# Kernel optimization log

Hardware: AMD Instinct MI355X
Metric: run time of the kernel (lower is better)

Reference implementation:

```python
import jax, jax.numpy as jnp
import numpy as np

K = 512   # cardinality of each hidden source
O = 8     # n_out per party
NS = 3    # number of sources (triangle network)


def setup_inputs() -> dict:
    key = jax.random.key(0)
    k1, k2 = jax.random.split(key)
    n_pred = NS * K + 3 * K * K * O
    y_pred = jax.random.uniform(k1, (1, n_pred), dtype=jnp.float32)
    y_true = jax.random.uniform(k2, (O ** 3,), dtype=jnp.float32)
    y_true = y_true / jnp.sum(y_true)  # a proper target distribution
    return {"y_pred": y_pred, "y_true": y_true}


def _distribution(y_pred):
    # sources block: [NS, K] source probability tables
    srcs = y_pred[0, :NS * K].reshape(NS, K)
    pf = y_pred[0, NS * K:]
    sz = K * K * O
    # party response tensors, indexed by the two source symbols the party sees
    A = pf[:sz].reshape(K, K, O)          # A sees (beta, gamma) -> (j, k)
    B = pf[sz:2 * sz].reshape(K, K, O)    # B sees (gamma, alpha) -> (k, i)
    C = pf[2 * sz:].reshape(K, K, O)      # C sees (alpha, beta) -> (i, j)
    Pa, Pb, Pc = srcs[0], srcs[1], srcs[2]
    # prob[x,y,z] = sum_{i,j,k} Pa[i] Pb[j] Pc[k] A[j,k,x] B[k,i,y] C[i,j,z]
    Aw = A * Pb[:, None, None] * Pc[None, :, None]   # [j,k,x]
    Bw = B * Pa[None, :, None]                        # [k,i,y]
    T = jnp.einsum('jkx,kiy->ijxy', Aw, Bw)           # contract k; [K,K,O,O]
    probs = jnp.einsum('ijxy,ijz->xyz', T, C)         # contract i,j; [O,O,O]
    return probs.reshape(-1)


def reference(y_pred, y_true):
    probs = _distribution(y_pred)
    log_p = jnp.log(jnp.clip(probs, 1e-10, 1.0))
    d = jnp.sum(y_true * (jnp.log(y_true + 1e-10) - log_p))
    return (d, probs)
```

## Files before the change

### kernel.cpp

```cpp
#include <hip/hip_runtime.h>
#include <hip/hip_bf16.h>
#include <stdint.h>

#define KD 512
#define OD 8
#define SZ (KD*KD*OD)
#define PLANE (KD*KD)

typedef short v8s __attribute__((ext_vector_type(8)));
typedef float v4f __attribute__((ext_vector_type(4)));

static __device__ __forceinline__ unsigned short f2bf(float f) {
    union { float f; unsigned int u; } v; v.f = f;
    unsigned int u = v.u;
    unsigned int r = u + 0x7FFF + ((u >> 16) & 1);
    return (unsigned short)(r >> 16);
}


__global__ __launch_bounds__(256) void pack_kernel(const float* __restrict__ yp,
                                                   unsigned short* __restrict__ Wbf,
                                                   unsigned short* __restrict__ Xbf,
                                                   float* __restrict__ probs_acc) {
    __shared__ unsigned short lds[8 * 32 * 32];
    const float* Pa = yp;
    const float* Pb = yp + KD;
    const float* Pc = yp + 2 * KD;
    const float* A  = yp + 3 * KD;
    const float* B  = A + SZ;
    const int b = blockIdx.x;
    const int t = threadIdx.x;

    if (b == 0) { probs_acc[t] = 0.0f; probs_acc[t + 256] = 0.0f; }

    if (b < 256) {
        #pragma unroll
        for (int jj = 0; jj < 2; ++jj) {
            const int j = b * 2 + jj;
            const float pb = Pb[j];
            const int k0 = 2 * t;
            const float4* src = (const float4*)(A + ((size_t)j * KD + k0) * 8);
            float av[16];
            ((float4*)av)[0] = src[0];
            ((float4*)av)[1] = src[1];
            ((float4*)av)[2] = src[2];
            ((float4*)av)[3] = src[3];
            const float s0 = pb * Pc[k0];
            const float s1 = pb * Pc[k0 + 1];
            const size_t fo = (size_t)(k0 >> 5) * 16384 + (size_t)(j >> 4) * 512
                            + (size_t)((k0 >> 3) & 3) * 128 + (j & 15) * 8 + (k0 & 7);
            #pragma unroll
            for (int x = 0; x < 8; ++x) {
                ushort2 w;
                w.x = f2bf(av[x] * s0);
                w.y = f2bf(av[8 + x] * s1);
                *(ushort2*)(Wbf + (size_t)x * PLANE + fo) = w;
            }
        }
    } else {
        const int tb = b - 256;
        const int k0 = (tb / 16) * 32;
        const int i0 = (tb % 16) * 32;
        char* ldsb = (char*)lds;
        #pragma unroll
        for (int p = 0; p < 4; ++p) {
            const int idx = t + p * 256;
            const int dk = idx >> 5;
            const int di = idx & 31;
            const float pa = Pa[i0 + di];
            const float4* src = (const float4*)(B + ((size_t)(k0 + dk) * KD + (i0 + di)) * 8);
            float bv[8];
            ((float4*)bv)[0] = src[0];
            ((float4*)bv)[1] = src[1];
            const int swz = (di & 7) << 4;
            #pragma unroll
            for (int y = 0; y < 8; ++y)
                *(unsigned short*)(ldsb + (y * 32 + di) * 64 + ((dk * 2) ^ swz)) =
                    f2bf(bv[y] * pa);
        }
        __syncthreads();
        #pragma unroll
        for (int p = 0; p < 4; ++p) {
            const int c = t + p * 256;
            const int y = c >> 7;
            const int rem = c & 127;
            const int di = rem >> 2;
            const int dk8 = (rem & 3) * 8;
            uint4 v = *(const uint4*)(ldsb + (y * 32 + di) * 64 + ((dk8 * 2) ^ ((di & 7) << 4)));
            const size_t fo = (size_t)(k0 >> 5) * 16384 + (size_t)((i0 + di) >> 4) * 512
                            + (size_t)(dk8 >> 3) * 128 + (di & 15) * 8;
            *(uint4*)(Xbf + (size_t)y * PLANE + fo) = v;
        }
    }
}

__global__ __launch_bounds__(256, 4) void gemm_kernel(const float* __restrict__ yp,
                                                      const unsigned short* __restrict__ Wbf,
                                                      const unsigned short* __restrict__ Xbf,
                                                      float* __restrict__ probs_acc) {
    __shared__ float red[4][32];

    const int bid = blockIdx.x;
    const int xcd = bid & 7;
    const int local = bid >> 3;
    const int tl = local >> 4;
    const int group = local & 15;
    const int i_t = ((xcd >> 1) << 1) | (tl >> 2);
    const int j_t = ((xcd & 1) << 2) | (tl & 3);
    const int i0 = i_t * 64, j0 = j_t * 64;
    const int x0 = (group >> 2) * 2, y0 = (group & 3) * 2;

    const int t = threadIdx.x;
    const int w = t >> 6;
    const int l = t & 63;
    const int wm = w >> 1, wn = w & 1;
    const int lm = l & 15, quad = l >> 4;

    const unsigned short* aP[2];
    const unsigned short* bP[2];
    #pragma unroll
    for (int dy = 0; dy < 2; ++dy)
        aP[dy] = Xbf + (size_t)(y0 + dy) * PLANE
               + (size_t)((i0 + wm * 32) >> 4) * 512 + l * 8;
    #pragma unroll
    for (int dx = 0; dx < 2; ++dx)
        bP[dx] = Wbf + (size_t)(x0 + dx) * PLANE
               + (size_t)((j0 + wn * 32) >> 4) * 512 + l * 8;

    v4f acc[2][2][2][2];
    #pragma unroll
    for (int a = 0; a < 2; ++a)
      #pragma unroll
      for (int bb = 0; bb < 2; ++bb)
        #pragma unroll
        for (int c = 0; c < 2; ++c)
          #pragma unroll
          for (int d = 0; d < 2; ++d)
            acc[a][bb][c][d] = (v4f){0.f, 0.f, 0.f, 0.f};

    #pragma unroll 4
    for (int kt = 0; kt < 16; ++kt) {
        const int kof = kt * 16384;
        v8s aF[2][2], bF[2][2];
        #pragma unroll
        for (int dy = 0; dy < 2; ++dy)
            #pragma unroll
            for (int mt = 0; mt < 2; ++mt)
                aF[dy][mt] = *(const v8s*)(aP[dy] + kof + mt * 512);
        #pragma unroll
        for (int dx = 0; dx < 2; ++dx)
            #pragma unroll
            for (int nt = 0; nt < 2; ++nt)
                bF[dx][nt] = *(const v8s*)(bP[dx] + kof + nt * 512);
        #pragma unroll
        for (int dy = 0; dy < 2; ++dy)
            #pragma unroll
            for (int dx = 0; dx < 2; ++dx)
                #pragma unroll
                for (int mt = 0; mt < 2; ++mt)
                    #pragma unroll
                    for (int nt = 0; nt < 2; ++nt)
                        acc[dy][dx][mt][nt] = __builtin_amdgcn_mfma_f32_16x16x32_bf16(
                            aF[dy][mt], bF[dx][nt], acc[dy][dx][mt][nt], 0, 0, 0);
    }

    const float* Cp = yp + 3 * KD + 2 * (size_t)SZ;
    float zacc[2][2][8];
    #pragma unroll
    for (int dy = 0; dy < 2; ++dy)
      #pragma unroll
      for (int dx = 0; dx < 2; ++dx)
        #pragma unroll
        for (int z = 0; z < 8; ++z) zacc[dy][dx][z] = 0.f;

    #pragma unroll
    for (int mt = 0; mt < 2; ++mt) {
        #pragma unroll
        for (int nt = 0; nt < 2; ++nt) {
            #pragma unroll
            for (int r = 0; r < 4; ++r) {
                const int gi = i0 + wm * 32 + mt * 16 + quad * 4 + r;
                const int gj = j0 + wn * 32 + nt * 16 + lm;
                const float4* cp = (const float4*)(Cp + ((size_t)gi * KD + gj) * 8);
                const float4 c0 = cp[0], c1 = cp[1];
                #pragma unroll
                for (int dy = 0; dy < 2; ++dy) {
                    #pragma unroll
                    for (int dx = 0; dx < 2; ++dx) {
                        const float tv = acc[dy][dx][mt][nt][r];
                        zacc[dy][dx][0] += tv * c0.x; zacc[dy][dx][1] += tv * c0.y;
                        zacc[dy][dx][2] += tv * c0.z; zacc[dy][dx][3] += tv * c0.w;
                        zacc[dy][dx][4] += tv * c1.x; zacc[dy][dx][5] += tv * c1.y;
                        zacc[dy][dx][6] += tv * c1.z; zacc[dy][dx][7] += tv * c1.w;
                    }
                }
            }
        }
    }
    #pragma unroll
    for (int dy = 0; dy < 2; ++dy)
      #pragma unroll
      for (int dx = 0; dx < 2; ++dx)
        #pragma unroll
        for (int z = 0; z < 8; ++z) {
            float v = zacc[dy][dx][z];
            for (int off = 32; off > 0; off >>= 1)
                v += __shfl_xor(v, off, 64);
            zacc[dy][dx][z] = v;
        }
    if (l == 0) {
        #pragma unroll
        for (int dy = 0; dy < 2; ++dy)
          #pragma unroll
          for (int dx = 0; dx < 2; ++dx)
            #pragma unroll
            for (int z = 0; z < 8; ++z)
                red[w][(dy * 2 + dx) * 8 + z] = zacc[dy][dx][z];
    }
    __syncthreads();
    if (t < 32) {
        const float s = red[0][t] + red[1][t] + red[2][t] + red[3][t];
        const int p = t >> 3;
        const int dy = p >> 1, dx = p & 1, z = t & 7;
        atomicAdd(&probs_acc[((x0 + dx) * 8 + (y0 + dy)) * 8 + z], s);
    }
}

__global__ __launch_bounds__(512) void finalize_kernel(const float* __restrict__ probs_acc,
                                                       const float* __restrict__ y_true,
                                                       float* __restrict__ out) {
    __shared__ float red[8];
    const int t = threadIdx.x;
    const float p = probs_acc[t];
    out[1 + t] = p;
    const float ytv = y_true[t];
    const float pc = fminf(fmaxf(p, 1e-10f), 1.0f);
    float term = ytv * (logf(ytv + 1e-10f) - logf(pc));
    for (int off = 32; off > 0; off >>= 1)
        term += __shfl_xor(term, off, 64);
    if ((t & 63) == 0) red[t >> 6] = term;
    __syncthreads();
    if (t == 0) {
        float s = 0.f;
        #pragma unroll
        for (int i = 0; i < 8; ++i) s += red[i];
        out[0] = s;
    }
}

extern "C" void kernel_launch(void* const* d_in, const int* in_sizes, int n_in,
                              void* d_out, int out_size, void* d_ws, size_t ws_size,
                              hipStream_t stream) {
    const float* yp = (const float*)d_in[0];
    const float* yt = (const float*)d_in[1];
    float* out = (float*)d_out;

    unsigned short* Wbf = (unsigned short*)d_ws;
    unsigned short* Xbf = Wbf + (size_t)8 * PLANE;
    float* probs_acc = (float*)(Xbf + (size_t)8 * PLANE);

    pack_kernel<<<512, 256, 0, stream>>>(yp, Wbf, Xbf, probs_acc);
    gemm_kernel<<<1024, 256, 0, stream>>>(yp, Wbf, Xbf, probs_acc);
    finalize_kernel<<<1, 512, 0, stream>>>(probs_acc, yt, out);
}
```

Baseline: 104.9 us.

## Stage GEMM operands through double-buffered LDS with async global-to-LDS loads

The GEMM kernel now uses 512-thread blocks with 128x128 tiles, so there are 256 blocks instead of 1024. Each block cooperatively streams its A/B fragments into a two-stage LDS ring using global_load_lds, and waits with vmcnt and barriers. Each wave computes a larger 64x32 sub-tile, and setprio is raised around the MFMA bursts. The aim is to cut redundant global fragment loads and overlap memory with MFMA work. The cost is more barriers, 64KB of LDS per block and fewer blocks for the 256 CUs.

```diff
diff --git a/kernel.cpp b/kernel.cpp
--- a/kernel.cpp
+++ b/kernel.cpp
@@ -9,12 +9,25 @@
 
 typedef short v8s __attribute__((ext_vector_type(8)));
 typedef float v4f __attribute__((ext_vector_type(4)));
+
+#define GLOBAL_AS __attribute__((address_space(1)))
+#define LDS_AS __attribute__((address_space(3)))
 
 static __device__ __forceinline__ unsigned short f2bf(float f) {
     union { float f; unsigned int u; } v; v.f = f;
     unsigned int u = v.u;
     unsigned int r = u + 0x7FFF + ((u >> 16) & 1);
     return (unsigned short)(r >> 16);
+}
+
+static __device__ __forceinline__ void async16(const unsigned short* g, unsigned short* l) {
+    __builtin_amdgcn_global_load_lds((const GLOBAL_AS void*)g, (LDS_AS void*)l, 16, 0, 0);
+}
+
+static __device__ __forceinline__ void bar() {
+    __builtin_amdgcn_sched_barrier(0);
+    __builtin_amdgcn_s_barrier();
+    __builtin_amdgcn_sched_barrier(0);
 }
 
 
@@ -94,74 +107,96 @@
     }
 }
 
-__global__ __launch_bounds__(256, 4) void gemm_kernel(const float* __restrict__ yp,
+__global__ __launch_bounds__(512, 2) void gemm_kernel(const float* __restrict__ yp,
                                                       const unsigned short* __restrict__ Wbf,
                                                       const unsigned short* __restrict__ Xbf,
                                                       float* __restrict__ probs_acc) {
-    __shared__ float red[4][32];
+    __shared__ unsigned short S[2][32 * 512];
+    __shared__ float red[8][32];
 
     const int bid = blockIdx.x;
     const int xcd = bid & 7;
     const int local = bid >> 3;
     const int tl = local >> 4;
     const int group = local & 15;
-    const int i_t = ((xcd >> 1) << 1) | (tl >> 2);
-    const int j_t = ((xcd & 1) << 2) | (tl & 3);
-    const int i0 = i_t * 64, j0 = j_t * 64;
+    const int i_t = xcd >> 1;
+    const int j_t = ((xcd & 1) << 1) | tl;
+    const int i0 = i_t * 128, j0 = j_t * 128;
     const int x0 = (group >> 2) * 2, y0 = (group & 3) * 2;
 
     const int t = threadIdx.x;
     const int w = t >> 6;
     const int l = t & 63;
-    const int wm = w >> 1, wn = w & 1;
+    const int wm = w >> 2, wn = w & 3;
     const int lm = l & 15, quad = l >> 4;
 
-    const unsigned short* aP[2];
-    const unsigned short* bP[2];
-    #pragma unroll
-    for (int dy = 0; dy < 2; ++dy)
-        aP[dy] = Xbf + (size_t)(y0 + dy) * PLANE
-               + (size_t)((i0 + wm * 32) >> 4) * 512 + l * 8;
-    #pragma unroll
-    for (int dx = 0; dx < 2; ++dx)
-        bP[dx] = Wbf + (size_t)(x0 + dx) * PLANE
-               + (size_t)((j0 + wn * 32) >> 4) * 512 + l * 8;
-
-    v4f acc[2][2][2][2];
+    const unsigned short* gq[4];
+    #pragma unroll
+    for (int q = 0; q < 4; ++q) {
+        const int idx = w * 4 + q;
+        const int tile = idx >> 3;
+        const int rt = idx & 7;
+        if (tile < 2)
+            gq[q] = Xbf + (size_t)(y0 + tile) * PLANE + (size_t)(i0 / 16 + rt) * 512 + l * 8;
+        else
+            gq[q] = Wbf + (size_t)(x0 + (tile - 2)) * PLANE + (size_t)(j0 / 16 + rt) * 512 + l * 8;
+    }
+    const int sbase = (w * 4) * 512;
+
+    v4f acc[2][2][4][2];
     #pragma unroll
     for (int a = 0; a < 2; ++a)
       #pragma unroll
       for (int bb = 0; bb < 2; ++bb)
         #pragma unroll
-        for (int c = 0; c < 2; ++c)
+        for (int c = 0; c < 4; ++c)
           #pragma unroll
           for (int d = 0; d < 2; ++d)
             acc[a][bb][c][d] = (v4f){0.f, 0.f, 0.f, 0.f};
 
-    #pragma unroll 4
-    for (int kt = 0; kt < 16; ++kt) {
-        const int kof = kt * 16384;
-        v8s aF[2][2], bF[2][2];
+    #pragma unroll
+    for (int q = 0; q < 4; ++q) async16(gq[q], &S[0][sbase + q * 512]);
+    #pragma unroll
+    for (int q = 0; q < 4; ++q) async16(gq[q] + 16384, &S[1][sbase + q * 512]);
+    asm volatile("s_waitcnt vmcnt(4)" ::: "memory");
+    bar();
+
+    for (int kc = 0; kc < 16; ++kc) {
+        const int cur = kc & 1;
+        v8s aF[2][4], bF[2][2];
         #pragma unroll
         for (int dy = 0; dy < 2; ++dy)
             #pragma unroll
-            for (int mt = 0; mt < 2; ++mt)
-                aF[dy][mt] = *(const v8s*)(aP[dy] + kof + mt * 512);
+            for (int mt = 0; mt < 4; ++mt)
+                aF[dy][mt] = *(const v8s*)&S[cur][(dy * 8 + wm * 4 + mt) * 512 + l * 8];
         #pragma unroll
         for (int dx = 0; dx < 2; ++dx)
             #pragma unroll
             for (int nt = 0; nt < 2; ++nt)
-                bF[dx][nt] = *(const v8s*)(bP[dx] + kof + nt * 512);
+                bF[dx][nt] = *(const v8s*)&S[cur][((2 + dx) * 8 + wn * 2 + nt) * 512 + l * 8];
+        __builtin_amdgcn_s_setprio(1);
         #pragma unroll
         for (int dy = 0; dy < 2; ++dy)
             #pragma unroll
             for (int dx = 0; dx < 2; ++dx)
                 #pragma unroll
-                for (int mt = 0; mt < 2; ++mt)
+                for (int mt = 0; mt < 4; ++mt)
                     #pragma unroll
                     for (int nt = 0; nt < 2; ++nt)
                         acc[dy][dx][mt][nt] = __builtin_amdgcn_mfma_f32_16x16x32_bf16(
                             aF[dy][mt], bF[dx][nt], acc[dy][dx][mt][nt], 0, 0, 0);
+        __builtin_amdgcn_s_setprio(0);
+        bar();
+        if (kc + 2 < 16) {
+            const size_t kb = (size_t)(kc + 2) * 16384;
+            #pragma unroll
+            for (int q = 0; q < 4; ++q) async16(gq[q] + kb, &S[cur][sbase + q * 512]);
+        }
+        if (kc < 15) {
+            if (kc + 2 < 16) asm volatile("s_waitcnt vmcnt(4)" ::: "memory");
+            else             asm volatile("s_waitcnt vmcnt(0)" ::: "memory");
+            bar();
+        }
     }
 
     const float* Cp = yp + 3 * KD + 2 * (size_t)SZ;
@@ -174,12 +209,12 @@
         for (int z = 0; z < 8; ++z) zacc[dy][dx][z] = 0.f;
 
     #pragma unroll
-    for (int mt = 0; mt < 2; ++mt) {
+    for (int mt = 0; mt < 4; ++mt) {
         #pragma unroll
         for (int nt = 0; nt < 2; ++nt) {
             #pragma unroll
             for (int r = 0; r < 4; ++r) {
-                const int gi = i0 + wm * 32 + mt * 16 + quad * 4 + r;
+                const int gi = i0 + wm * 64 + mt * 16 + quad * 4 + r;
                 const int gj = j0 + wn * 32 + nt * 16 + lm;
                 const float4* cp = (const float4*)(Cp + ((size_t)gi * KD + gj) * 8);
                 const float4 c0 = cp[0], c1 = cp[1];
@@ -219,7 +254,9 @@
     }
     __syncthreads();
     if (t < 32) {
-        const float s = red[0][t] + red[1][t] + red[2][t] + red[3][t];
+        float s = 0.f;
+        #pragma unroll
+        for (int ww = 0; ww < 8; ++ww) s += red[ww][t];
         const int p = t >> 3;
         const int dy = p >> 1, dx = p & 1, z = t & 7;
         atomicAdd(&probs_acc[((x0 + dx) * 8 + (y0 + dy)) * 8 + z], s);
@@ -260,6 +297,6 @@
     float* probs_acc = (float*)(Xbf + (size_t)8 * PLANE);
 
     pack_kernel<<<512, 256, 0, stream>>>(yp, Wbf, Xbf, probs_acc);
-    gemm_kernel<<<1024, 256, 0, stream>>>(yp, Wbf, Xbf, probs_acc);
+    gemm_kernel<<<256, 512, 0, stream>>>(yp, Wbf, Xbf, probs_acc);
     finalize_kernel<<<1, 512, 0, stream>>>(probs_acc, yt, out);
 }
```

Measured after the change: 102.4 us. 2.5% less time.
